# Kernel tuning notes

Hardware: AMD Instinct MI355X
Metric: run time of the kernel (lower is better)

## Reference

```python
import jax, jax.numpy as jnp
import numpy as np

N = 50000
E = 800000
D = 128
DOUT = 128
KEEP_SCALE = 2.0  # 1 / (1 - drop_rate), drop_rate = 0.5


def setup_inputs() -> dict:
    key = jax.random.key(0)
    k1, k2, k3, k4, k5, k6 = jax.random.split(key, 6)
    X = jax.random.normal(k1, (N, D), dtype=jnp.float32)
    W = jax.random.normal(k2, (2 * D, DOUT), dtype=jnp.float32) * (1.0 / np.sqrt(2 * D))
    b = jax.random.normal(k3, (DOUT,), dtype=jnp.float32) * 0.01
    src = jax.random.randint(k4, (E,), 0, N, dtype=jnp.int32)
    dst = jax.random.randint(k5, (E,), 0, N, dtype=jnp.int32)
    drop_mask = jax.random.randint(k6, (N, DOUT), 0, 2, dtype=jnp.int32)
    return {"X": X, "W": W, "b": b, "src": src, "dst": dst, "drop_mask": drop_mask}


def reference(X, W, b, src, dst, drop_mask):
    # v2v mean aggregation: X_nbr[i] = mean_{(j->i) in E} X[j]
    nbr_sum = jax.ops.segment_sum(X[src], dst, num_segments=N)        # [N, D]
    deg = jax.ops.segment_sum(jnp.ones((E,), X.dtype), dst, num_segments=N)  # [N]
    X_nbr = nbr_sum / jnp.maximum(deg, 1.0)[:, None]
    # concat + linear + relu + dropout (deterministic mask, train-mode scaling)
    H = jnp.concatenate([X, X_nbr], axis=1)                           # [N, 2D]
    out = jax.nn.relu(H @ W + b)
    out = out * (drop_mask.astype(out.dtype) * KEEP_SCALE)
    return out
```

## Files before the change

### kernel.cpp

```cpp
#include <hip/hip_runtime.h>

#define NN 50000
#define ND 50048
#define NW 6256
#define NE 800000
#define CHUNKS 32
#define EPC 25000
#define CAP 56
#define NTILE 3125
#define CVT_UNITS 1600000
#define CVT_BLOCKS 1563

typedef __attribute__((ext_vector_type(8))) short short8;
typedef __attribute__((ext_vector_type(4))) float f32x4;
typedef __attribute__((ext_vector_type(4))) unsigned int u32x4;
typedef __attribute__((ext_vector_type(2))) unsigned int u32x2;


__device__ __forceinline__ unsigned f2bf(float f) {
  unsigned u = __builtin_bit_cast(unsigned, f);
  return (u + 0x7fffu + ((u >> 16) & 1u)) >> 16;
}
__device__ __forceinline__ float bflo(unsigned u) {
  return __builtin_bit_cast(float, u << 16);
}
__device__ __forceinline__ float bfhi(unsigned u) {
  return __builtin_bit_cast(float, u & 0xffff0000u);
}

__global__ __launch_bounds__(1024) void k_rankconv(const int* __restrict__ dst,
                                                   const float* __restrict__ W,
                                                   const float* __restrict__ X,
                                                   unsigned char* __restrict__ rank,
                                                   unsigned int* __restrict__ chunkcnt,
                                                   u32x4* __restrict__ Wfrag,
                                                   u32x2* __restrict__ Xbf2) {
  int tid = threadIdx.x;
  int c = blockIdx.x;
  if (c >= CHUNKS) {
    int i = (c - CHUNKS) * 1024 + tid;
    if (i < CVT_UNITS) {
      f32x4 v = ((const f32x4*)X)[i];
      u32x2 o;
      o[0] = f2bf(v[0]) | (f2bf(v[1]) << 16);
      o[1] = f2bf(v[2]) | (f2bf(v[3]) << 16);
      Xbf2[i] = o;
    } else if (i < CVT_UNITS + 32) {
      Xbf2[i] = (u32x2){0u, 0u};
    }
    return;
  }
  __shared__ unsigned int pack[NW];
  if (tid < 128) {
    int s = c * 128 + tid;
    int lane = s & 63;
    int t = (s >> 6) & 7;
    int kb = s >> 9;
    int col = t * 16 + (lane & 15);
    int k0 = kb * 32 + (lane >> 4) * 8;
    u32x4 o;
#pragma unroll
    for (int p = 0; p < 4; ++p) {
      unsigned lo = f2bf(W[(k0 + 2 * p) * 128 + col]);
      unsigned hi = f2bf(W[(k0 + 2 * p + 1) * 128 + col]);
      o[p] = lo | (hi << 16);
    }
    Wfrag[s] = o;
  }
  for (int w = tid; w < NW; w += 1024) pack[w] = 0;
  __syncthreads();
  int ebase = c * EPC;
  for (int i = tid; i < EPC; i += 1024) {
    int e = ebase + i;
    int d = dst[e];
    unsigned sh = (unsigned)(d & 7) * 4u;
    unsigned old = atomicAdd(&pack[d >> 3], 1u << sh);
    rank[e] = (unsigned char)((old >> sh) & 15u);
  }
  __syncthreads();
  for (int w = tid; w < NW; w += 1024) chunkcnt[(size_t)c * NW + w] = pack[w];
}

__global__ __launch_bounds__(64) void k_base(const unsigned int* __restrict__ chunkcnt,
                                             unsigned char* __restrict__ chunkbase,
                                             unsigned int* __restrict__ deg) {
  int d = blockIdx.x * 64 + threadIdx.x;
  if (d >= NN) return;
  int w = d >> 3;
  unsigned sh = (unsigned)(d & 7) * 4u;
  unsigned cnts[CHUNKS];
#pragma unroll
  for (int c = 0; c < CHUNKS; ++c) cnts[c] = chunkcnt[(size_t)c * NW + w];
  unsigned run = 0;
#pragma unroll
  for (int c = 0; c < CHUNKS; ++c) {
    chunkbase[(size_t)c * ND + d] = (unsigned char)run;
    run += (cnts[c] >> sh) & 15u;
  }
  deg[d] = run;
}

__global__ __launch_bounds__(256) void k_place(const int* __restrict__ src,
                                               const int* __restrict__ dst,
                                               const unsigned char* __restrict__ rank,
                                               const unsigned char* __restrict__ chunkbase,
                                               unsigned short* __restrict__ slots) {
  int e = blockIdx.x * 256 + threadIdx.x;
  if (e >= NE) return;
  int c = e / EPC;
  int d = dst[e];
  int pos = (int)chunkbase[(size_t)c * ND + d] + (int)rank[e];
  if (pos < CAP) slots[d * CAP + pos] = (unsigned short)src[e];
}

__global__ __launch_bounds__(256) void k_fused(const unsigned short* __restrict__ Xbf,
                                               const unsigned int* __restrict__ deg,
                                               const unsigned short* __restrict__ slots,
                                               const u32x4* __restrict__ Wfrag,
                                               const float* __restrict__ b,
                                               const int* __restrict__ mask,
                                               float* __restrict__ out) {
  __shared__ unsigned short nbr[16 * 136];
  int lane = threadIdx.x & 63;
  int wid = threadIdx.x >> 6;
  int tile = blockIdx.x;
  int g = lane >> 4;
  int il = lane & 15;
  const u32x4* Xb4 = (const u32x4*)Xbf;

  int node = tile * 16 + wid * 4 + g;
  int dg = (int)deg[node];
  int m = min(dg, CAP);
  int mmax = m;
  mmax = max(mmax, __shfl_xor(mmax, 16, 64));
  mmax = max(mmax, __shfl_xor(mmax, 32, 64));
  const unsigned short* sl = slots + node * CAP;
  int s0 = sl[il];
  int s1 = sl[16 + il];
  int s2 = sl[32 + il];
  int s3 = sl[min(48 + il, CAP - 1)];
  float acc[8];
#pragma unroll
  for (int k = 0; k < 8; ++k) acc[k] = 0.f;

#define ACC8(v)                                       \
  {                                                   \
    acc[0] += bflo(v[0]); acc[1] += bfhi(v[0]);       \
    acc[2] += bflo(v[1]); acc[3] += bfhi(v[1]);       \
    acc[4] += bflo(v[2]); acc[5] += bfhi(v[2]);       \
    acc[6] += bflo(v[3]); acc[7] += bfhi(v[3]);       \
  }
#define GATHER4(sj, E0)                                     \
  if ((E0) < mmax) {                                        \
    int a0_ = __shfl(sj, g * 16 + ((E0) & 15) + 0, 64);     \
    int a1_ = __shfl(sj, g * 16 + ((E0) & 15) + 1, 64);     \
    int a2_ = __shfl(sj, g * 16 + ((E0) & 15) + 2, 64);     \
    int a3_ = __shfl(sj, g * 16 + ((E0) & 15) + 3, 64);     \
    a0_ = ((E0) + 0 < m) ? a0_ : NN;                        \
    a1_ = ((E0) + 1 < m) ? a1_ : NN;                        \
    a2_ = ((E0) + 2 < m) ? a2_ : NN;                        \
    a3_ = ((E0) + 3 < m) ? a3_ : NN;                        \
    u32x4 v0_ = Xb4[(size_t)a0_ * 16 + il];                 \
    u32x4 v1_ = Xb4[(size_t)a1_ * 16 + il];                 \
    u32x4 v2_ = Xb4[(size_t)a2_ * 16 + il];                 \
    u32x4 v3_ = Xb4[(size_t)a3_ * 16 + il];                 \
    ACC8(v0_); ACC8(v1_); ACC8(v2_); ACC8(v3_);             \
  }

  GATHER4(s0, 0)  GATHER4(s0, 4)  GATHER4(s0, 8)  GATHER4(s0, 12)
  GATHER4(s1, 16) GATHER4(s1, 20) GATHER4(s1, 24) GATHER4(s1, 28)
  GATHER4(s2, 32) GATHER4(s2, 36) GATHER4(s2, 40) GATHER4(s2, 44)
  GATHER4(s3, 48) GATHER4(s3, 52)
#undef GATHER4
#undef ACC8

  {
    float inv = 1.0f / (float)max(dg, 1);
    int r = wid * 4 + g;
    u32x4 o;
#pragma unroll
    for (int p = 0; p < 4; ++p)
      o[p] = f2bf(acc[2 * p] * inv) | (f2bf(acc[2 * p + 1] * inv) << 16);
    *(u32x4*)(&nbr[r * 136 + il * 8]) = o;
  }
  __syncthreads();

  int t0 = wid * 2;
  int t1 = wid * 2 + 1;
  int arow = tile * 16 + il;
  f32x4 c0 = (f32x4){0.f, 0.f, 0.f, 0.f};
  f32x4 c1 = (f32x4){0.f, 0.f, 0.f, 0.f};
#pragma unroll
  for (int kb = 0; kb < 4; ++kb) {
    short8 a = __builtin_bit_cast(short8, Xb4[(size_t)arow * 16 + kb * 4 + g]);
    short8 w0 = __builtin_bit_cast(short8, Wfrag[(kb * 8 + t0) * 64 + lane]);
    short8 w1 = __builtin_bit_cast(short8, Wfrag[(kb * 8 + t1) * 64 + lane]);
    c0 = __builtin_amdgcn_mfma_f32_16x16x32_bf16(a, w0, c0, 0, 0, 0);
    c1 = __builtin_amdgcn_mfma_f32_16x16x32_bf16(a, w1, c1, 0, 0, 0);
  }
#pragma unroll
  for (int kb = 0; kb < 4; ++kb) {
    short8 a = *(const short8*)(&nbr[il * 136 + kb * 32 + g * 8]);
    short8 w0 = __builtin_bit_cast(short8, Wfrag[((kb + 4) * 8 + t0) * 64 + lane]);
    short8 w1 = __builtin_bit_cast(short8, Wfrag[((kb + 4) * 8 + t1) * 64 + lane]);
    c0 = __builtin_amdgcn_mfma_f32_16x16x32_bf16(a, w0, c0, 0, 0, 0);
    c1 = __builtin_amdgcn_mfma_f32_16x16x32_bf16(a, w1, c1, 0, 0, 0);
  }

  float b0 = b[t0 * 16 + il];
  float b1 = b[t1 * 16 + il];
  int orow = tile * 16 + g * 4;
#pragma unroll
  for (int rg = 0; rg < 4; ++rg) {
    size_t i0 = (size_t)(orow + rg) * 128 + t0 * 16 + il;
    size_t i1 = (size_t)(orow + rg) * 128 + t1 * 16 + il;
    float v0 = fmaxf(c0[rg] + b0, 0.f) * (2.0f * (float)mask[i0]);
    float v1 = fmaxf(c1[rg] + b1, 0.f) * (2.0f * (float)mask[i1]);
    out[i0] = v0;
    out[i1] = v1;
  }
}

extern "C" void kernel_launch(void* const* d_in, const int* in_sizes, int n_in,
                              void* d_out, int out_size, void* d_ws, size_t ws_size,
                              hipStream_t stream) {
  (void)in_sizes; (void)n_in; (void)out_size; (void)ws_size;
  const float* X = (const float*)d_in[0];
  const float* W = (const float*)d_in[1];
  const float* b = (const float*)d_in[2];
  const int* src = (const int*)d_in[3];
  const int* dst = (const int*)d_in[4];
  const int* mask = (const int*)d_in[5];
  float* out = (float*)d_out;

  char* ws = (char*)d_ws;
  u32x4* Wfrag = (u32x4*)ws;
  unsigned int* deg = (unsigned int*)(ws + 65536);
  unsigned short* slots = (unsigned short*)(ws + 265728);
  u32x2* Xbf2 = (u32x2*)(ws + 5865728);
  const unsigned short* Xbf = (const unsigned short*)(ws + 5865728);
  unsigned char* rank = (unsigned char*)(ws + 18666240);
  unsigned int* chunkcnt = (unsigned int*)(ws + 19466240);
  unsigned char* chunkbase = (unsigned char*)(ws + 20267008);

  k_rankconv<<<CHUNKS + CVT_BLOCKS, 1024, 0, stream>>>(dst, W, X, rank, chunkcnt, Wfrag, Xbf2);
  k_base<<<(NN + 63) / 64, 64, 0, stream>>>(chunkcnt, chunkbase, deg);
  k_place<<<(NE + 255) / 256, 256, 0, stream>>>(src, dst, rank, chunkbase, slots);
  k_fused<<<NTILE, 256, 0, stream>>>(Xbf, deg, slots, Wfrag, b, mask, out);
}
```

Measured before the change: 71.95 us.

## Gather neighbor features from an FP8 copy of X and software-pipeline the gather loads

Adds an FP8 (e4m3) copy of X alongside the bf16 copy in the conversion kernel, and the neighbor gather now reads 8-byte FP8 rows instead of 16-byte bf16 rows. This halves gather traffic, which is the dominant random-access cost. The gather is restructured into double-buffered load/accumulate blocks, and the mask and bias loads are hoisted ahead of the gather so their latency overlaps. In exchange, the aggregated features lose precision (3-bit mantissa), which may threaten tolerance. The extra FP8 write also adds a little work to the conversion pass.

Result: faster. 67.81 us (-5.8%).

```diff
diff --git a/kernel.cpp b/kernel.cpp
--- a/kernel.cpp
+++ b/kernel.cpp
@@ -13,6 +13,7 @@
 
 typedef __attribute__((ext_vector_type(8))) short short8;
 typedef __attribute__((ext_vector_type(4))) float f32x4;
+typedef __attribute__((ext_vector_type(2))) float f32x2;
 typedef __attribute__((ext_vector_type(4))) unsigned int u32x4;
 typedef __attribute__((ext_vector_type(2))) unsigned int u32x2;
 
@@ -21,12 +22,39 @@
   unsigned u = __builtin_bit_cast(unsigned, f);
   return (u + 0x7fffu + ((u >> 16) & 1u)) >> 16;
 }
-__device__ __forceinline__ float bflo(unsigned u) {
-  return __builtin_bit_cast(float, u << 16);
-}
-__device__ __forceinline__ float bfhi(unsigned u) {
-  return __builtin_bit_cast(float, u & 0xffff0000u);
-}
+
+#if defined(__has_builtin) && __has_builtin(__builtin_amdgcn_cvt_pk_fp8_f32) && \
+    __has_builtin(__builtin_amdgcn_cvt_pk_f32_fp8)
+#define FP8_HW 1
+#else
+#define FP8_HW 0
+#endif
+
+#if !FP8_HW
+__device__ __forceinline__ unsigned f2fp8(float x) {
+  unsigned u = __builtin_bit_cast(unsigned, x);
+  unsigned s = (u >> 24) & 0x80u;
+  float a = __builtin_bit_cast(float, u & 0x7fffffffu);
+  if (a < 0.015625f) {
+    unsigned q = (unsigned)(a * 512.0f + 0.5f);
+    return s | (q == 8u ? 0x08u : q);
+  }
+  if (a >= 448.0f) return s | 0x7Eu;
+  unsigned v = u & 0x7fffffffu;
+  v = v + 0x0007FFFFu + ((v >> 20) & 1u);
+  unsigned e = (v >> 23) - 120u;
+  if (e >= 16u) return s | 0x7Eu;
+  return s | (e << 3) | ((v >> 20) & 7u);
+}
+__device__ __forceinline__ float fp82f(unsigned b) {
+  unsigned s = (b & 0x80u) << 24;
+  unsigned e = (b >> 3) & 15u;
+  unsigned m = b & 7u;
+  unsigned mag = e ? ((e + 120u) << 23) | (m << 20)
+                   : __builtin_bit_cast(unsigned, (float)m * 0.001953125f);
+  return __builtin_bit_cast(float, s | mag);
+}
+#endif
 
 __global__ __launch_bounds__(1024) void k_rankconv(const int* __restrict__ dst,
                                                    const float* __restrict__ W,
@@ -34,7 +62,8 @@
                                                    unsigned char* __restrict__ rank,
                                                    unsigned int* __restrict__ chunkcnt,
                                                    u32x4* __restrict__ Wfrag,
-                                                   u32x2* __restrict__ Xbf2) {
+                                                   u32x2* __restrict__ Xbf2,
+                                                   unsigned int* __restrict__ Xf8w) {
   int tid = threadIdx.x;
   int c = blockIdx.x;
   if (c >= CHUNKS) {
@@ -45,8 +74,17 @@
       o[0] = f2bf(v[0]) | (f2bf(v[1]) << 16);
       o[1] = f2bf(v[2]) | (f2bf(v[3]) << 16);
       Xbf2[i] = o;
+      unsigned p8;
+#if FP8_HW
+      p8 = __builtin_amdgcn_cvt_pk_fp8_f32(v[0], v[1], 0, false);
+      p8 = __builtin_amdgcn_cvt_pk_fp8_f32(v[2], v[3], p8, true);
+#else
+      p8 = f2fp8(v[0]) | (f2fp8(v[1]) << 8) | (f2fp8(v[2]) << 16) | (f2fp8(v[3]) << 24);
+#endif
+      Xf8w[i] = p8;
     } else if (i < CVT_UNITS + 32) {
       Xbf2[i] = (u32x2){0u, 0u};
+      Xf8w[i] = 0u;
     }
     return;
   }
@@ -114,6 +152,7 @@
 }
 
 __global__ __launch_bounds__(256) void k_fused(const unsigned short* __restrict__ Xbf,
+                                               const unsigned char* __restrict__ Xf8,
                                                const unsigned int* __restrict__ deg,
                                                const unsigned short* __restrict__ slots,
                                                const u32x4* __restrict__ Wfrag,
@@ -127,6 +166,9 @@
   int g = lane >> 4;
   int il = lane & 15;
   const u32x4* Xb4 = (const u32x4*)Xbf;
+  const u32x2* X8 = (const u32x2*)Xf8;
+  int t0 = wid * 2;
+  int t1 = wid * 2 + 1;
 
   int node = tile * 16 + wid * 4 + g;
   int dg = (int)deg[node];
@@ -143,36 +185,85 @@
 #pragma unroll
   for (int k = 0; k < 8; ++k) acc[k] = 0.f;
 
-#define ACC8(v)                                       \
-  {                                                   \
-    acc[0] += bflo(v[0]); acc[1] += bfhi(v[0]);       \
-    acc[2] += bflo(v[1]); acc[3] += bfhi(v[1]);       \
-    acc[4] += bflo(v[2]); acc[5] += bfhi(v[2]);       \
-    acc[6] += bflo(v[3]); acc[7] += bfhi(v[3]);       \
-  }
-#define GATHER4(sj, E0)                                     \
-  if ((E0) < mmax) {                                        \
-    int a0_ = __shfl(sj, g * 16 + ((E0) & 15) + 0, 64);     \
-    int a1_ = __shfl(sj, g * 16 + ((E0) & 15) + 1, 64);     \
-    int a2_ = __shfl(sj, g * 16 + ((E0) & 15) + 2, 64);     \
-    int a3_ = __shfl(sj, g * 16 + ((E0) & 15) + 3, 64);     \
-    a0_ = ((E0) + 0 < m) ? a0_ : NN;                        \
-    a1_ = ((E0) + 1 < m) ? a1_ : NN;                        \
-    a2_ = ((E0) + 2 < m) ? a2_ : NN;                        \
-    a3_ = ((E0) + 3 < m) ? a3_ : NN;                        \
-    u32x4 v0_ = Xb4[(size_t)a0_ * 16 + il];                 \
-    u32x4 v1_ = Xb4[(size_t)a1_ * 16 + il];                 \
-    u32x4 v2_ = Xb4[(size_t)a2_ * 16 + il];                 \
-    u32x4 v3_ = Xb4[(size_t)a3_ * 16 + il];                 \
-    ACC8(v0_); ACC8(v1_); ACC8(v2_); ACC8(v3_);             \
-  }
-
-  GATHER4(s0, 0)  GATHER4(s0, 4)  GATHER4(s0, 8)  GATHER4(s0, 12)
-  GATHER4(s1, 16) GATHER4(s1, 20) GATHER4(s1, 24) GATHER4(s1, 28)
-  GATHER4(s2, 32) GATHER4(s2, 36) GATHER4(s2, 40) GATHER4(s2, 44)
-  GATHER4(s3, 48) GATHER4(s3, 52)
-#undef GATHER4
+#define SLOT(e)                                                              \
+  ({                                                                         \
+    int t_ = __shfl((e) < 16 ? s0 : (e) < 32 ? s1 : (e) < 48 ? s2 : s3,      \
+                    g * 16 + ((e) & 15), 64);                                \
+    ((e) < m) ? t_ : NN;                                                     \
+  })
+#define LOADBLK(va, E0)                         \
+  if ((E0) < mmax) {                            \
+    int a0_ = SLOT((E0) + 0);                   \
+    int a1_ = SLOT((E0) + 1);                   \
+    int a2_ = SLOT((E0) + 2);                   \
+    int a3_ = SLOT((E0) + 3);                   \
+    va[0] = X8[(size_t)a0_ * 16 + il];          \
+    va[1] = X8[(size_t)a1_ * 16 + il];          \
+    va[2] = X8[(size_t)a2_ * 16 + il];          \
+    va[3] = X8[(size_t)a3_ * 16 + il];          \
+  }
+#if FP8_HW
+#define ACC8(v)                                                      \
+  {                                                                  \
+    f32x2 p0_ = __builtin_amdgcn_cvt_pk_f32_fp8((int)v[0], false);   \
+    f32x2 p1_ = __builtin_amdgcn_cvt_pk_f32_fp8((int)v[0], true);    \
+    f32x2 p2_ = __builtin_amdgcn_cvt_pk_f32_fp8((int)v[1], false);   \
+    f32x2 p3_ = __builtin_amdgcn_cvt_pk_f32_fp8((int)v[1], true);    \
+    acc[0] += p0_[0]; acc[1] += p0_[1];                              \
+    acc[2] += p1_[0]; acc[3] += p1_[1];                              \
+    acc[4] += p2_[0]; acc[5] += p2_[1];                              \
+    acc[6] += p3_[0]; acc[7] += p3_[1];                              \
+  }
+#else
+#define ACC8(v)                                                      \
+  {                                                                  \
+    acc[0] += fp82f(v[0] & 255u);                                    \
+    acc[1] += fp82f((v[0] >> 8) & 255u);                             \
+    acc[2] += fp82f((v[0] >> 16) & 255u);                            \
+    acc[3] += fp82f(v[0] >> 24);                                     \
+    acc[4] += fp82f(v[1] & 255u);                                    \
+    acc[5] += fp82f((v[1] >> 8) & 255u);                             \
+    acc[6] += fp82f((v[1] >> 16) & 255u);                            \
+    acc[7] += fp82f(v[1] >> 24);                                     \
+  }
+#endif
+#define ACCBLK(va, E0)                          \
+  if ((E0) < mmax) {                            \
+    ACC8(va[0]); ACC8(va[1]);                   \
+    ACC8(va[2]); ACC8(va[3]);                   \
+  }
+
+  u32x2 vA[4], vB[4];
+  LOADBLK(vA, 0)
+  LOADBLK(vB, 4)
+
+  int mk0[4], mk1[4];
+#pragma unroll
+  for (int rg = 0; rg < 4; ++rg) {
+    mk0[rg] = mask[(size_t)(tile * 16 + g * 4 + rg) * 128 + t0 * 16 + il];
+    mk1[rg] = mask[(size_t)(tile * 16 + g * 4 + rg) * 128 + t1 * 16 + il];
+  }
+  float b0 = b[t0 * 16 + il];
+  float b1 = b[t1 * 16 + il];
+
+  ACCBLK(vA, 0)  LOADBLK(vA, 8)
+  ACCBLK(vB, 4)  LOADBLK(vB, 12)
+  ACCBLK(vA, 8)  LOADBLK(vA, 16)
+  ACCBLK(vB, 12) LOADBLK(vB, 20)
+  ACCBLK(vA, 16) LOADBLK(vA, 24)
+  ACCBLK(vB, 20) LOADBLK(vB, 28)
+  ACCBLK(vA, 24) LOADBLK(vA, 32)
+  ACCBLK(vB, 28) LOADBLK(vB, 36)
+  ACCBLK(vA, 32) LOADBLK(vA, 40)
+  ACCBLK(vB, 36) LOADBLK(vB, 44)
+  ACCBLK(vA, 40) LOADBLK(vA, 48)
+  ACCBLK(vB, 44) LOADBLK(vB, 52)
+  ACCBLK(vA, 48)
+  ACCBLK(vB, 52)
+#undef SLOT
+#undef LOADBLK
 #undef ACC8
+#undef ACCBLK
 
   {
     float inv = 1.0f / (float)max(dg, 1);
@@ -185,8 +276,6 @@
   }
   __syncthreads();
 
-  int t0 = wid * 2;
-  int t1 = wid * 2 + 1;
   int arow = tile * 16 + il;
   f32x4 c0 = (f32x4){0.f, 0.f, 0.f, 0.f};
   f32x4 c1 = (f32x4){0.f, 0.f, 0.f, 0.f};
@@ -207,17 +296,13 @@
     c1 = __builtin_amdgcn_mfma_f32_16x16x32_bf16(a, w1, c1, 0, 0, 0);
   }
 
-  float b0 = b[t0 * 16 + il];
-  float b1 = b[t1 * 16 + il];
   int orow = tile * 16 + g * 4;
 #pragma unroll
   for (int rg = 0; rg < 4; ++rg) {
     size_t i0 = (size_t)(orow + rg) * 128 + t0 * 16 + il;
     size_t i1 = (size_t)(orow + rg) * 128 + t1 * 16 + il;
-    float v0 = fmaxf(c0[rg] + b0, 0.f) * (2.0f * (float)mask[i0]);
-    float v1 = fmaxf(c1[rg] + b1, 0.f) * (2.0f * (float)mask[i1]);
-    out[i0] = v0;
-    out[i1] = v1;
+    out[i0] = fmaxf(c0[rg] + b0, 0.f) * (2.0f * (float)mk0[rg]);
+    out[i1] = fmaxf(c1[rg] + b1, 0.f) * (2.0f * (float)mk1[rg]);
   }
 }
 
@@ -237,14 +322,17 @@
   u32x4* Wfrag = (u32x4*)ws;
   unsigned int* deg = (unsigned int*)(ws + 65536);
   unsigned short* slots = (unsigned short*)(ws + 265728);
-  u32x2* Xbf2 = (u32x2*)(ws + 5865728);
-  const unsigned short* Xbf = (const unsigned short*)(ws + 5865728);
-  unsigned char* rank = (unsigned char*)(ws + 18666240);
-  unsigned int* chunkcnt = (unsigned int*)(ws + 19466240);
-  unsigned char* chunkbase = (unsigned char*)(ws + 20267008);
-
-  k_rankconv<<<CHUNKS + CVT_BLOCKS, 1024, 0, stream>>>(dst, W, X, rank, chunkcnt, Wfrag, Xbf2);
+  unsigned int* Xf8w = (unsigned int*)(ws + 5865728);
+  const unsigned char* Xf8 = (const unsigned char*)(ws + 5865728);
+  u32x2* Xbf2 = (u32x2*)(ws + 12265984);
+  const unsigned short* Xbf = (const unsigned short*)(ws + 12265984);
+  unsigned char* rank = (unsigned char*)(ws + 25066240);
+  unsigned int* chunkcnt = (unsigned int*)(ws + 25866240);
+  unsigned char* chunkbase = (unsigned char*)(ws + 26667008);
+
+  k_rankconv<<<CHUNKS + CVT_BLOCKS, 1024, 0, stream>>>(dst, W, X, rank, chunkcnt, Wfrag,
+                                                       Xbf2, Xf8w);
   k_base<<<(NN + 63) / 64, 64, 0, stream>>>(chunkcnt, chunkbase, deg);
   k_place<<<(NE + 255) / 256, 256, 0, stream>>>(src, dst, rank, chunkbase, slots);
-  k_fused<<<NTILE, 256, 0, stream>>>(Xbf, deg, slots, Wfrag, b, mask, out);
-}
+  k_fused<<<NTILE, 256, 0, stream>>>(Xbf, Xf8, deg, slots, Wfrag, b, mask, out);
+}
```
